# Performance work log

Measured on AMD Instinct MI355X. Metric: run time of the kernel, lower is better.

## Reference

```python
import jax, jax.numpy as jnp
from jax import lax
import numpy as np

N_BITS = 12
BATCH = 4_194_304


def setup_inputs() -> dict:
    key = jax.random.key(0)
    kA, kB = jax.random.split(key)
    # Binary spike inputs (0.0 / 1.0) as the SNN logic gates expect.
    A = jax.random.randint(kA, (BATCH, N_BITS), 0, 2).astype(jnp.float32)
    B = jax.random.randint(kB, (BATCH, N_BITS), 0, 2).astype(jnp.float32)
    return {"A": A, "B": B}


def reference(A, B):
    """12-bit ripple-borrow subtractor A - B using soft boolean gate algebra.

    Gate math on {0,1} spikes: XOR(a,b)=a+b-2ab, AND=ab, OR=a+b-ab, NOT=1-a.
    Bit 11 is the LSB (loop runs i=11..0), Bin defaults to 0.
    Returns (diff [..., 12], final_borrow [..., 1]).
    """

    def step(borrow, ab):  # borrow: [batch], a/b: [batch]
        a, b = ab
        t1 = a + b - 2.0 * a * b            # xor1: a ^ b
        diff = t1 + borrow - 2.0 * t1 * borrow  # xor2: t1 ^ borrow
        na = 1.0 - a                         # not a
        term1 = na * b                       # and1
        term2 = na * borrow                  # and2
        term3 = b * borrow                   # and3
        o1 = term1 + term2 - term1 * term2   # or1
        new_borrow = o1 + term3 - o1 * term3 # or2
        return new_borrow, diff

    # Reorder bits so scan walks LSB (index 11) -> MSB (index 0).
    a_seq = jnp.moveaxis(A, -1, 0)[::-1]  # [12, batch...]
    b_seq = jnp.moveaxis(B, -1, 0)[::-1]
    borrow0 = jnp.zeros_like(A[..., 0])

    borrow, diffs = lax.scan(step, borrow0, (a_seq, b_seq))
    diffs = jnp.moveaxis(diffs[::-1], 0, -1)  # back to [..., 12], index 0 = MSB
    return diffs, borrow[..., None]
```

## Files before the change

kernel.cpp:

```cpp
#include <hip/hip_runtime.h>


#define ROWS 256
#define LDS_STRIDE 13

__global__ __launch_bounds__(256) void Subtractor12Bit_kernel(
    const float4* __restrict__ A4,
    const float4* __restrict__ B4,
    float4* __restrict__ D4,
    float* __restrict__ Borrow,
    int batch)
{
    __shared__ float sa[ROWS * LDS_STRIDE];
    __shared__ float sb[ROWS * LDS_STRIDE];

    const int t = threadIdx.x;
    const int rowBase = blockIdx.x * ROWS;
    const int gbase = blockIdx.x * (ROWS * 3);

    const bool full = (rowBase + ROWS) <= batch;

    #pragma unroll
    for (int k = 0; k < 3; ++k) {
        const int f = t + 256 * k;
        const int r = f / 3;
        const int c = (f % 3) * 4;
        const int addr = r * LDS_STRIDE + c;
        if (full || (rowBase + r) < batch) {
            const float4 a = A4[gbase + f];
            const float4 b = B4[gbase + f];
            sa[addr + 0] = a.x; sa[addr + 1] = a.y; sa[addr + 2] = a.z; sa[addr + 3] = a.w;
            sb[addr + 0] = b.x; sb[addr + 1] = b.y; sb[addr + 2] = b.z; sb[addr + 3] = b.w;
        }
    }
    __syncthreads();

    const int row = rowBase + t;
    if (full || row < batch) {
        const int base = t * LDS_STRIDE;
        unsigned ua = 0u, ub = 0u;
        #pragma unroll
        for (int j = 0; j < 12; ++j) {
            ua |= (unsigned)(sa[base + j] > 0.5f) << (11 - j);
            ub |= (unsigned)(sb[base + j] > 0.5f) << (11 - j);
        }
        const unsigned diff = (ua - ub) & 0xFFFu;
        Borrow[row] = (ub > ua) ? 1.0f : 0.0f;
        #pragma unroll
        for (int j = 0; j < 12; ++j)
            sa[base + j] = (float)((diff >> (11 - j)) & 1u);
    }
    __syncthreads();

    #pragma unroll
    for (int k = 0; k < 3; ++k) {
        const int f = t + 256 * k;
        const int r = f / 3;
        const int c = (f % 3) * 4;
        const int addr = r * LDS_STRIDE + c;
        if (full || (rowBase + r) < batch) {
            float4 d;
            d.x = sa[addr + 0]; d.y = sa[addr + 1]; d.z = sa[addr + 2]; d.w = sa[addr + 3];
            D4[gbase + f] = d;
        }
    }
}

extern "C" void kernel_launch(void* const* d_in, const int* in_sizes, int n_in,
                              void* d_out, int out_size, void* d_ws, size_t ws_size,
                              hipStream_t stream) {
    const float* A = (const float*)d_in[0];
    const float* B = (const float*)d_in[1];
    float* out = (float*)d_out;

    const int batch = in_sizes[0] / 12;
    float* diffs = out;
    float* borrow = out + (size_t)batch * 12;

    const int grid = (batch + ROWS - 1) / ROWS;
    Subtractor12Bit_kernel<<<grid, 256, 0, stream>>>(
        (const float4*)A, (const float4*)B, (float4*)diffs, borrow, batch);
}
```

Before: 456.7 us.

## Drop LDS staging; load each row's 48 bytes directly per thread and bit-extract

Removes the shared-memory transpose and its two barriers. Each thread now loads its own row as three 16-byte vectors from A and B and gets each bit from the float exponent bit (bit 23) instead of comparing floats. It writes the output bits as 0.0f/1.0f patterns by masking. The per-thread loads use a 48-byte stride, so coalescing across the wave is weaker than with the staged layout, but every full cache line is still consumed by neighbouring threads. Reading bit 23 is only correct when the inputs are exactly 0.0 or 1.0.

```diff
diff --git a/kernel.cpp b/kernel.cpp
--- a/kernel.cpp
+++ b/kernel.cpp
@@ -1,69 +1,61 @@
 #include <hip/hip_runtime.h>
 
 
-#define ROWS 256
-#define LDS_STRIDE 13
-
-__global__ __launch_bounds__(256) void Subtractor12Bit_kernel(
-    const float4* __restrict__ A4,
-    const float4* __restrict__ B4,
-    float4* __restrict__ D4,
+__global__ __launch_bounds__(256, 8) void Subtractor12Bit_kernel(
+    const uint4* __restrict__ A4,
+    const uint4* __restrict__ B4,
+    uint4* __restrict__ D4,
     float* __restrict__ Borrow,
     int batch)
 {
-    __shared__ float sa[ROWS * LDS_STRIDE];
-    __shared__ float sb[ROWS * LDS_STRIDE];
+    const int row = blockIdx.x * 256 + threadIdx.x;
+    if (row >= batch) return;
+    const int base = row * 3;
 
-    const int t = threadIdx.x;
-    const int rowBase = blockIdx.x * ROWS;
-    const int gbase = blockIdx.x * (ROWS * 3);
+    const uint4 a0 = A4[base + 0];
+    const uint4 a1 = A4[base + 1];
+    const uint4 a2 = A4[base + 2];
+    const uint4 b0 = B4[base + 0];
+    const uint4 b1 = B4[base + 1];
+    const uint4 b2 = B4[base + 2];
 
-    const bool full = (rowBase + ROWS) <= batch;
+    const unsigned ua =
+        (((a0.x >> 23) & 1u) << 11) | (((a0.y >> 23) & 1u) << 10) |
+        (((a0.z >> 23) & 1u) <<  9) | (((a0.w >> 23) & 1u) <<  8) |
+        (((a1.x >> 23) & 1u) <<  7) | (((a1.y >> 23) & 1u) <<  6) |
+        (((a1.z >> 23) & 1u) <<  5) | (((a1.w >> 23) & 1u) <<  4) |
+        (((a2.x >> 23) & 1u) <<  3) | (((a2.y >> 23) & 1u) <<  2) |
+        (((a2.z >> 23) & 1u) <<  1) | (((a2.w >> 23) & 1u)      );
+    const unsigned ub =
+        (((b0.x >> 23) & 1u) << 11) | (((b0.y >> 23) & 1u) << 10) |
+        (((b0.z >> 23) & 1u) <<  9) | (((b0.w >> 23) & 1u) <<  8) |
+        (((b1.x >> 23) & 1u) <<  7) | (((b1.y >> 23) & 1u) <<  6) |
+        (((b1.z >> 23) & 1u) <<  5) | (((b1.w >> 23) & 1u) <<  4) |
+        (((b2.x >> 23) & 1u) <<  3) | (((b2.y >> 23) & 1u) <<  2) |
+        (((b2.z >> 23) & 1u) <<  1) | (((b2.w >> 23) & 1u)      );
 
-    #pragma unroll
-    for (int k = 0; k < 3; ++k) {
-        const int f = t + 256 * k;
-        const int r = f / 3;
-        const int c = (f % 3) * 4;
-        const int addr = r * LDS_STRIDE + c;
-        if (full || (rowBase + r) < batch) {
-            const float4 a = A4[gbase + f];
-            const float4 b = B4[gbase + f];
-            sa[addr + 0] = a.x; sa[addr + 1] = a.y; sa[addr + 2] = a.z; sa[addr + 3] = a.w;
-            sb[addr + 0] = b.x; sb[addr + 1] = b.y; sb[addr + 2] = b.z; sb[addr + 3] = b.w;
-        }
-    }
-    __syncthreads();
+    const unsigned diff = (ua - ub) & 0xFFFu;
 
-    const int row = rowBase + t;
-    if (full || row < batch) {
-        const int base = t * LDS_STRIDE;
-        unsigned ua = 0u, ub = 0u;
-        #pragma unroll
-        for (int j = 0; j < 12; ++j) {
-            ua |= (unsigned)(sa[base + j] > 0.5f) << (11 - j);
-            ub |= (unsigned)(sb[base + j] > 0.5f) << (11 - j);
-        }
-        const unsigned diff = (ua - ub) & 0xFFFu;
-        Borrow[row] = (ub > ua) ? 1.0f : 0.0f;
-        #pragma unroll
-        for (int j = 0; j < 12; ++j)
-            sa[base + j] = (float)((diff >> (11 - j)) & 1u);
-    }
-    __syncthreads();
+    Borrow[row] = (ub > ua) ? 1.0f : 0.0f;
 
-    #pragma unroll
-    for (int k = 0; k < 3; ++k) {
-        const int f = t + 256 * k;
-        const int r = f / 3;
-        const int c = (f % 3) * 4;
-        const int addr = r * LDS_STRIDE + c;
-        if (full || (rowBase + r) < batch) {
-            float4 d;
-            d.x = sa[addr + 0]; d.y = sa[addr + 1]; d.z = sa[addr + 2]; d.w = sa[addr + 3];
-            D4[gbase + f] = d;
-        }
-    }
+    const unsigned ONE = 0x3F800000u;
+    uint4 d0, d1, d2;
+    d0.x = ONE & (0u - ((diff >> 11) & 1u));
+    d0.y = ONE & (0u - ((diff >> 10) & 1u));
+    d0.z = ONE & (0u - ((diff >>  9) & 1u));
+    d0.w = ONE & (0u - ((diff >>  8) & 1u));
+    d1.x = ONE & (0u - ((diff >>  7) & 1u));
+    d1.y = ONE & (0u - ((diff >>  6) & 1u));
+    d1.z = ONE & (0u - ((diff >>  5) & 1u));
+    d1.w = ONE & (0u - ((diff >>  4) & 1u));
+    d2.x = ONE & (0u - ((diff >>  3) & 1u));
+    d2.y = ONE & (0u - ((diff >>  2) & 1u));
+    d2.z = ONE & (0u - ((diff >>  1) & 1u));
+    d2.w = ONE & (0u - ( diff        & 1u));
+
+    D4[base + 0] = d0;
+    D4[base + 1] = d1;
+    D4[base + 2] = d2;
 }
 
 extern "C" void kernel_launch(void* const* d_in, const int* in_sizes, int n_in,
@@ -77,7 +69,7 @@
     float* diffs = out;
     float* borrow = out + (size_t)batch * 12;
 
-    const int grid = (batch + ROWS - 1) / ROWS;
+    const int grid = (batch + 255) / 256;
     Subtractor12Bit_kernel<<<grid, 256, 0, stream>>>(
-        (const float4*)A, (const float4*)B, (float4*)diffs, borrow, batch);
+        (const uint4*)A, (const uint4*)B, (uint4*)diffs, borrow, batch);
 }
```

After: 460.0 us. Within noise of the previous version (+0.7%).
